# Kernel tuning notes

Hardware: AMD Instinct MI355X
Metric: run time of the kernel (lower is better)

Reference implementation:

```python
import jax, jax.numpy as jnp
import numpy as np

N = 1_000_000   # total nodes
D = 128         # hidden_dim
B = 1024        # number of graphs (segments)
E = 2_000_000   # edges (unused by forward math, kept for signature fidelity)
EPS = 1e-16     # PyG softmax denominator epsilon


def setup_inputs() -> dict:
    key = jax.random.key(0)
    k1, k2, k3, k4 = jax.random.split(key, 4)
    x = jax.random.normal(k1, (N, D), dtype=jnp.float32)
    edge_index = jax.random.randint(k2, (2, E), 0, N, dtype=jnp.int32)
    batch = jnp.sort(jax.random.randint(k3, (N,), 0, B, dtype=jnp.int32))
    # Linear(hidden_dim, 1) parameters
    W = jax.random.normal(k4, (1, D), dtype=jnp.float32) * (1.0 / np.sqrt(D))
    b = jnp.zeros((1,), dtype=jnp.float32)
    return {"x": x, "edge_index": edge_index, "batch": batch, "W": W, "b": b}


def reference(x, edge_index, batch, W, b):
    # scores = Linear(x).squeeze(-1)  -> [N]
    scores = (x @ W.T + b)[:, 0]
    # pyg_softmax: segment-wise numerically-stable softmax over `batch`
    seg_max = jax.ops.segment_max(scores, batch, num_segments=B)          # [B]
    ex = jnp.exp(scores - seg_max[batch])                                  # [N]
    seg_sum = jax.ops.segment_sum(ex, batch, num_segments=B)              # [B]
    attn = ex / (seg_sum[batch] + EPS)                                     # [N]
    # global_add_pool of attention-weighted features -> [B, D]
    gx = jax.ops.segment_sum(x * attn[:, None], batch, num_segments=B)
    return gx
```

## Files before the change

### kernel.cpp

```cpp
#include <hip/hip_runtime.h>
#include <math.h>


#define DIM 128
#define NEG_HUGE (-3.0e38f)

__global__ void seg_offsets_kernel(const int* __restrict__ batch,
                                   int* __restrict__ off, int N, int B) {
    int i = blockIdx.x * blockDim.x + threadIdx.x;
    if (i >= N) return;
    int bi = batch[i];
    int bp = (i == 0) ? -1 : batch[i - 1];
    for (int s = bp + 1; s <= bi; ++s) off[s] = i;
    if (i == N - 1) {
        for (int s = bi + 1; s <= B; ++s) off[s] = N;
    }
}

__global__ __launch_bounds__(256) void gap_online_kernel(
    const float* __restrict__ x,
    const int*   __restrict__ off,
    const float* __restrict__ W,
    const float* __restrict__ bias,
    float*       __restrict__ out)
{
    const int seg  = blockIdx.x;
    const int tid  = threadIdx.x;
    const int wave = tid >> 6;
    const int lane = tid & 63;
    const int half = lane >> 5;
    const int hl   = lane & 31;

    const int start = off[seg];
    const int end   = off[seg + 1];

    const float4 wv = ((const float4*)W)[hl];
    const float  b0 = bias[0];

    float  m = NEG_HUGE;
    float  l = 0.0f;
    float4 acc = make_float4(0.f, 0.f, 0.f, 0.f);

    int p = start + wave * 8;

    float4 xv[4];
    #pragma unroll
    for (int k = 0; k < 4; ++k) {
        int row = p + 2 * k + half;
        xv[k] = (row < end) ? ((const float4*)(x + (size_t)row * DIM))[hl]
                            : make_float4(0.f, 0.f, 0.f, 0.f);
    }

    for (; p < end; p += 32) {
        float4 xn[4];
        #pragma unroll
        for (int k = 0; k < 4; ++k) {
            int row = p + 32 + 2 * k + half;
            xn[k] = (row < end) ? ((const float4*)(x + (size_t)row * DIM))[hl]
                                : make_float4(0.f, 0.f, 0.f, 0.f);
        }

        float s[4];
        #pragma unroll
        for (int k = 0; k < 4; ++k)
            s[k] = xv[k].x * wv.x + xv[k].y * wv.y + xv[k].z * wv.z + xv[k].w * wv.w;

        #pragma unroll
        for (int offd = 16; offd > 0; offd >>= 1) {
            #pragma unroll
            for (int k = 0; k < 4; ++k)
                s[k] += __shfl_xor(s[k], offd, 64);
        }

        #pragma unroll
        for (int k = 0; k < 4; ++k) {
            int  row   = p + 2 * k + half;
            bool valid = row < end;
            float sk    = valid ? (s[k] + b0) : NEG_HUGE;
            float m_new = fmaxf(m, sk);
            float alpha = __expf(m - m_new);
            float w     = valid ? __expf(sk - m_new) : 0.0f;
            l     = l * alpha + w;
            acc.x = acc.x * alpha + w * xv[k].x;
            acc.y = acc.y * alpha + w * xv[k].y;
            acc.z = acc.z * alpha + w * xv[k].z;
            acc.w = acc.w * alpha + w * xv[k].w;
            m     = m_new;
            xv[k] = xn[k];
        }
    }

    __shared__ float sm[8];
    __shared__ float sl[8];
    __shared__ float sacc[8][DIM];

    const int sid = wave * 2 + half;
    sacc[sid][4 * hl + 0] = acc.x;
    sacc[sid][4 * hl + 1] = acc.y;
    sacc[sid][4 * hl + 2] = acc.z;
    sacc[sid][4 * hl + 3] = acc.w;
    if (hl == 0) { sm[sid] = m; sl[sid] = l; }
    __syncthreads();

    if (tid < DIM) {
        float m_tot = NEG_HUGE;
        #pragma unroll
        for (int h = 0; h < 8; ++h) m_tot = fmaxf(m_tot, sm[h]);
        float num = 0.0f, den = 0.0f;
        #pragma unroll
        for (int h = 0; h < 8; ++h) {
            float a = __expf(sm[h] - m_tot);
            num += sacc[h][tid] * a;
            den += sl[h] * a;
        }
        out[(size_t)seg * DIM + tid] = num / (den + 1e-16f);
    }
}

extern "C" void kernel_launch(void* const* d_in, const int* in_sizes, int n_in,
                              void* d_out, int out_size, void* d_ws, size_t ws_size,
                              hipStream_t stream) {
    const float* x     = (const float*)d_in[0];
    const int*   batch = (const int*)d_in[2];
    const float* W     = (const float*)d_in[3];
    const float* bias  = (const float*)d_in[4];
    float*       out   = (float*)d_out;

    const int N = in_sizes[2];
    const int B = out_size / DIM;

    int* off = (int*)d_ws;

    seg_offsets_kernel<<<(N + 255) / 256, 256, 0, stream>>>(batch, off, N, B);
    gap_online_kernel<<<B, 256, 0, stream>>>(x, off, W, bias, out);
}
```

Measured before the change: 666.8 us.

## Split each segment across eight blocks and merge partial softmax states

Each segment is now divided into eight chunks handled by separate blocks. Each block writes its partial max, denominator and weighted sum to workspace, and a new merge kernel combines them. This raises the block count from 1024 to 8192 so more memory parallelism is in flight on a bandwidth-bound 512MB read. The online-softmax update is also batched: one rescale per four rows instead of one per row, which cuts exp calls. The cost is an extra kernel launch and a small partial-result buffer.

```diff
diff --git a/kernel.cpp b/kernel.cpp
--- a/kernel.cpp
+++ b/kernel.cpp
@@ -3,6 +3,7 @@
 
 
 #define DIM 128
+#define CHUNKS 8
 #define NEG_HUGE (-3.0e38f)
 
 __global__ void seg_offsets_kernel(const int* __restrict__ batch,
@@ -17,22 +18,29 @@
     }
 }
 
-__global__ __launch_bounds__(256) void gap_online_kernel(
+__global__ __launch_bounds__(256) void gap_partial_kernel(
     const float* __restrict__ x,
     const int*   __restrict__ off,
     const float* __restrict__ W,
     const float* __restrict__ bias,
-    float*       __restrict__ out)
+    float*       __restrict__ pm,
+    float*       __restrict__ pl,
+    float*       __restrict__ pacc)
 {
-    const int seg  = blockIdx.x;
+    const int blk   = blockIdx.x;
+    const int seg   = blk >> 3;
+    const int chunk = blk & (CHUNKS - 1);
     const int tid  = threadIdx.x;
     const int wave = tid >> 6;
     const int lane = tid & 63;
     const int half = lane >> 5;
     const int hl   = lane & 31;
 
-    const int start = off[seg];
-    const int end   = off[seg + 1];
+    const int s0  = off[seg];
+    const int s1  = off[seg + 1];
+    const int len = s1 - s0;
+    const int start = s0 + (len * chunk) / CHUNKS;
+    const int end   = s0 + (len * (chunk + 1)) / CHUNKS;
 
     const float4 wv = ((const float4*)W)[hl];
     const float  b0 = bias[0];
@@ -72,22 +80,34 @@
                 s[k] += __shfl_xor(s[k], offd, 64);
         }
 
+        float sk[4];
+        float tm = m;
         #pragma unroll
         for (int k = 0; k < 4; ++k) {
-            int  row   = p + 2 * k + half;
-            bool valid = row < end;
-            float sk    = valid ? (s[k] + b0) : NEG_HUGE;
-            float m_new = fmaxf(m, sk);
-            float alpha = __expf(m - m_new);
-            float w     = valid ? __expf(sk - m_new) : 0.0f;
-            l     = l * alpha + w;
-            acc.x = acc.x * alpha + w * xv[k].x;
-            acc.y = acc.y * alpha + w * xv[k].y;
-            acc.z = acc.z * alpha + w * xv[k].z;
-            acc.w = acc.w * alpha + w * xv[k].w;
-            m     = m_new;
+            int row = p + 2 * k + half;
+            sk[k] = (row < end) ? (s[k] + b0) : NEG_HUGE;
+            tm = fmaxf(tm, sk[k]);
+        }
+        float alpha = __expf(m - tm);
+        float wsum = 0.0f;
+        float4 a2 = make_float4(0.f, 0.f, 0.f, 0.f);
+        #pragma unroll
+        for (int k = 0; k < 4; ++k) {
+            int  row = p + 2 * k + half;
+            float w  = (row < end) ? __expf(sk[k] - tm) : 0.0f;
+            wsum += w;
+            a2.x += w * xv[k].x;
+            a2.y += w * xv[k].y;
+            a2.z += w * xv[k].z;
+            a2.w += w * xv[k].w;
             xv[k] = xn[k];
         }
+        l     = l * alpha + wsum;
+        acc.x = acc.x * alpha + a2.x;
+        acc.y = acc.y * alpha + a2.y;
+        acc.z = acc.z * alpha + a2.z;
+        acc.w = acc.w * alpha + a2.w;
+        m     = tm;
     }
 
     __shared__ float sm[8];
@@ -113,8 +133,35 @@
             num += sacc[h][tid] * a;
             den += sl[h] * a;
         }
-        out[(size_t)seg * DIM + tid] = num / (den + 1e-16f);
+        pacc[(size_t)blk * DIM + tid] = num;
+        if (tid == 0) { pm[blk] = m_tot; pl[blk] = den; }
     }
+}
+
+__global__ __launch_bounds__(128) void gap_merge_kernel(
+    const float* __restrict__ pm,
+    const float* __restrict__ pl,
+    const float* __restrict__ pacc,
+    float*       __restrict__ out)
+{
+    const int seg = blockIdx.x;
+    const int d   = threadIdx.x;
+
+    float ms[CHUNKS];
+    float mt = NEG_HUGE;
+    #pragma unroll
+    for (int c = 0; c < CHUNKS; ++c) {
+        ms[c] = pm[seg * CHUNKS + c];
+        mt = fmaxf(mt, ms[c]);
+    }
+    float num = 0.0f, den = 0.0f;
+    #pragma unroll
+    for (int c = 0; c < CHUNKS; ++c) {
+        float a = __expf(ms[c] - mt);
+        num += pacc[(size_t)(seg * CHUNKS + c) * DIM + d] * a;
+        den += pl[seg * CHUNKS + c] * a;
+    }
+    out[(size_t)seg * DIM + d] = num / (den + 1e-16f);
 }
 
 extern "C" void kernel_launch(void* const* d_in, const int* in_sizes, int n_in,
@@ -129,8 +176,13 @@
     const int N = in_sizes[2];
     const int B = out_size / DIM;
 
-    int* off = (int*)d_ws;
+    int*   off = (int*)d_ws;
+    size_t offb = (((size_t)(B + 1) * sizeof(int)) + 255) & ~(size_t)255;
+    float* pm   = (float*)((char*)d_ws + offb);
+    float* pl   = pm + (size_t)B * CHUNKS;
+    float* pacc = pl + (size_t)B * CHUNKS;
 
     seg_offsets_kernel<<<(N + 255) / 256, 256, 0, stream>>>(batch, off, N, B);
-    gap_online_kernel<<<B, 256, 0, stream>>>(x, off, W, bias, out);
+    gap_partial_kernel<<<B * CHUNKS, 256, 0, stream>>>(x, off, W, bias, pm, pl, pacc);
+    gap_merge_kernel<<<B, 128, 0, stream>>>(pm, pl, pacc, out);
 }
```

Measured after the change: 664.9 us. No clear change (-0.3%).
